# Optimization experiments

Hardware: AMD Instinct MI355X
Metric: run time of the kernel (lower is better)

## Reference

```python
import jax, jax.numpy as jnp
import numpy as np

N_ATOMS = 50000
N_EDGES = 1600000
NAB = 128   # n_atom_basis
NRBF = 20   # n_rbf
NF = 128    # n_filters

LOG2 = float(np.log(2.0))

def shifted_softplus(x):
    return jax.nn.softplus(x) - LOG2

def setup_inputs() -> dict:
    key = jax.random.key(0)
    ks = jax.random.split(key, 16)
    x = jax.random.normal(ks[0], (N_ATOMS, NAB), dtype=jnp.float32)
    f_ij = jax.random.normal(ks[1], (N_EDGES, NRBF), dtype=jnp.float32)
    rcut_ij = jax.random.uniform(ks[2], (N_EDGES,), dtype=jnp.float32)
    idx_i = jnp.sort(jax.random.randint(ks[3], (N_EDGES,), 0, N_ATOMS))
    idx_j = jax.random.randint(ks[4], (N_EDGES,), 0, N_ATOMS)
    def xavier(k, shape):
        fan_in, fan_out = shape
        s = float(np.sqrt(6.0 / (fan_in + fan_out)))
        return jax.random.uniform(k, shape, dtype=jnp.float32, minval=-s, maxval=s)
    # in2f: Dense(NAB, NF, bias=False)
    W_in2f = xavier(ks[5], (NAB, NF))
    # filter_network: Dense(NRBF, NF, act=ssp), Dense(NF, NF)
    W_f1 = xavier(ks[6], (NRBF, NF)); b_f1 = jnp.zeros((NF,), jnp.float32)
    W_f2 = xavier(ks[7], (NF, NF));   b_f2 = jnp.zeros((NF,), jnp.float32)
    # f2out: Dense(NF, NAB, act=ssp), Dense(NAB, NAB)
    W_o1 = xavier(ks[8], (NF, NAB));  b_o1 = jnp.zeros((NAB,), jnp.float32)
    W_o2 = xavier(ks[9], (NAB, NAB)); b_o2 = jnp.zeros((NAB,), jnp.float32)
    return {"x": x, "f_ij": f_ij, "rcut_ij": rcut_ij, "idx_i": idx_i, "idx_j": idx_j,
            "W_in2f": W_in2f, "W_f1": W_f1, "b_f1": b_f1, "W_f2": W_f2, "b_f2": b_f2,
            "W_o1": W_o1, "b_o1": b_o1, "W_o2": W_o2, "b_o2": b_o2}

def reference(x, f_ij, rcut_ij, idx_i, idx_j,
              W_in2f, W_f1, b_f1, W_f2, b_f2, W_o1, b_o1, W_o2, b_o2):
    # in2f (no bias, no activation): [N, NF]
    h = x @ W_in2f
    # filter network on radial basis: [E, NF]
    Wij = shifted_softplus(f_ij @ W_f1 + b_f1) @ W_f2 + b_f2
    Wij = Wij * rcut_ij[:, None]
    # cfconv: gather neighbor features, modulate by filter, scatter-sum to centers
    x_ij = h[idx_j] * Wij                      # [E, NF]
    y = jax.ops.segment_sum(x_ij, idx_i, num_segments=N_ATOMS)  # [N, NF]
    # f2out
    out = shifted_softplus(y @ W_o1 + b_o1) @ W_o2 + b_o2       # [N, NAB]
    return out
```

## Files before the change

kernel.cpp:

```cpp
#include <hip/hip_runtime.h>
#include <math.h>

#define N_ATOMS 50000
#define N_EDGES 1600000
#define NRBF 20
#define TILE_E 32
#define N_TILES (N_EDGES / TILE_E)

typedef __attribute__((ext_vector_type(8))) short bf16x8;
typedef __attribute__((ext_vector_type(4))) float f32x4;

__device__ __forceinline__ float ssp(float v) {
    const float a = fabsf(v);
    const float e = exp2f(a * -1.4426950408889634f);
    const float l = log2f(1.0f + e);
    return fmaxf(v, 0.0f) + fmaf(l, 0.6931471805599453f, -0.6931471805599453f);
}
__device__ __forceinline__ unsigned short f2bf(float f) {
    unsigned int u = __float_as_uint(f);
    u += 0x7fff + ((u >> 16) & 1);
    return (unsigned short)(u >> 16);
}
__device__ __forceinline__ float bf2f(unsigned short b) {
    return __uint_as_float(((unsigned int)b) << 16);
}
__device__ __forceinline__ void lds_barrier() {
    __asm__ __volatile__("s_waitcnt lgkmcnt(0)\ns_barrier" ::: "memory");
}

template<bool SSP_ACT, bool BIAS>
__global__ __launch_bounds__(512) void rowgemm_mfma(
    const float* __restrict__ A, const float* __restrict__ W,
    const float* __restrict__ bias, float* __restrict__ C, int nrows)
{
    const int tid  = threadIdx.x;
    const int wave = tid >> 6, lane = tid & 63;
    const int l15  = lane & 15, quad = lane >> 4;
    const int rhalf = wave >> 2, cpair = wave & 3;
    const int r0 = rhalf * 16;
    const int ntiles = (nrows + 31) >> 5;
    const int stride = gridDim.x;

    int t = blockIdx.x;
    if (t >= ntiles) return;

    float av[4][8];
    {
        const int arow0 = t * 32 + r0 + l15;
        const int arow = (arow0 < nrows) ? arow0 : (nrows - 1);
        #pragma unroll
        for (int kk = 0; kk < 4; ++kk) {
            const float4 q0 = *(const float4*)(A + (size_t)arow * 128 + kk * 32 + quad * 8);
            const float4 q1 = *(const float4*)(A + (size_t)arow * 128 + kk * 32 + quad * 8 + 4);
            av[kk][0] = q0.x; av[kk][1] = q0.y; av[kk][2] = q0.z; av[kk][3] = q0.w;
            av[kk][4] = q1.x; av[kk][5] = q1.y; av[kk][6] = q1.z; av[kk][7] = q1.w;
        }
    }

    bf16x8 wh[2][4], wl[2][4];
    float br[2];
    #pragma unroll
    for (int ct = 0; ct < 2; ++ct) {
        const int c = cpair * 32 + ct * 16 + l15;
        br[ct] = BIAS ? bias[c] : 0.0f;
        #pragma unroll
        for (int kk = 0; kk < 4; ++kk) {
            #pragma unroll
            for (int j = 0; j < 8; ++j) {
                const int k = kk * 32 + quad * 8 + j;
                const float v = W[k * 128 + c];
                const unsigned short hb = f2bf(v);
                wh[ct][kk][j] = (short)hb;
                wl[ct][kk][j] = (short)f2bf(v - bf2f(hb));
            }
        }
    }

    while (true) {
        const int tn = t + stride;
        const bool more = (tn < ntiles);
        float avn[4][8];
        if (more) {
            const int arow0 = tn * 32 + r0 + l15;
            const int arow = (arow0 < nrows) ? arow0 : (nrows - 1);
            #pragma unroll
            for (int kk = 0; kk < 4; ++kk) {
                const float4 q0 = *(const float4*)(A + (size_t)arow * 128 + kk * 32 + quad * 8);
                const float4 q1 = *(const float4*)(A + (size_t)arow * 128 + kk * 32 + quad * 8 + 4);
                avn[kk][0] = q0.x; avn[kk][1] = q0.y; avn[kk][2] = q0.z; avn[kk][3] = q0.w;
                avn[kk][4] = q1.x; avn[kk][5] = q1.y; avn[kk][6] = q1.z; avn[kk][7] = q1.w;
            }
        }
        bf16x8 ah[4], al[4];
        #pragma unroll
        for (int kk = 0; kk < 4; ++kk) {
            #pragma unroll
            for (int j = 0; j < 8; ++j) {
                const unsigned short hb = f2bf(av[kk][j]);
                ah[kk][j] = (short)hb;
                al[kk][j] = (short)f2bf(av[kk][j] - bf2f(hb));
            }
        }
        #pragma unroll
        for (int ct = 0; ct < 2; ++ct) {
            f32x4 acc = {0.0f, 0.0f, 0.0f, 0.0f};
            #pragma unroll
            for (int kk = 0; kk < 4; ++kk) {
                acc = __builtin_amdgcn_mfma_f32_16x16x32_bf16(ah[kk], wh[ct][kk], acc, 0, 0, 0);
                acc = __builtin_amdgcn_mfma_f32_16x16x32_bf16(al[kk], wh[ct][kk], acc, 0, 0, 0);
                acc = __builtin_amdgcn_mfma_f32_16x16x32_bf16(ah[kk], wl[ct][kk], acc, 0, 0, 0);
            }
            const int c = cpair * 32 + ct * 16 + l15;
            #pragma unroll
            for (int r = 0; r < 4; ++r) {
                const int row = t * 32 + r0 + quad * 4 + r;
                if (row < nrows) {
                    float v = acc[r] + br[ct];
                    if (SSP_ACT) v = ssp(v);
                    C[(size_t)row * 128 + c] = v;
                }
            }
        }
        if (!more) break;
        #pragma unroll
        for (int kk = 0; kk < 4; ++kk)
            #pragma unroll
            for (int j = 0; j < 8; ++j) av[kk][j] = avn[kk][j];
        t = tn;
    }
}

__global__ __launch_bounds__(512, 2) void edge_mfma(
    const float* __restrict__ f_ij, const float* __restrict__ rcut,
    const int* __restrict__ idx_i, const int* __restrict__ idx_j,
    const float* __restrict__ h,
    const float* __restrict__ W1, const float* __restrict__ b1,
    const float* __restrict__ W2, const float* __restrict__ b2,
    float* __restrict__ y)
{
    __shared__ unsigned short sTH[32][136];
    __shared__ float sXT[128][33];

    const int tid  = threadIdx.x;
    const int wave = tid >> 6, lane = tid & 63;
    const int l15  = lane & 15, quad = lane >> 4;
    const int rhalf = wave >> 2, cpair = wave & 3;
    const int r0  = rhalf * 16;
    const int c0  = cpair * 32 + l15;
    const int rr  = r0 + quad * 4;
    const int col = tid & 127, qtr = tid >> 7;

    bf16x8 w1h[2];
    bf16x8 w2h[2][4];
    float b1r[2], b2r[2];
    #pragma unroll
    for (int ct = 0; ct < 2; ++ct) {
        const int c = c0 + ct * 16;
        b1r[ct] = b1[c];
        b2r[ct] = b2[c];
        #pragma unroll
        for (int j = 0; j < 8; ++j) {
            const int k = quad * 8 + j;
            w1h[ct][j] = (short)f2bf((k < NRBF) ? W1[k * 128 + c] : 0.0f);
        }
        #pragma unroll
        for (int kk = 0; kk < 4; ++kk)
            #pragma unroll
            for (int j = 0; j < 8; ++j)
                w2h[ct][kk][j] = (short)f2bf(W2[(kk * 32 + quad * 8 + j) * 128 + c]);
    }

    const int nb = gridDim.x;
    const int t0 = (int)(((long long)blockIdx.x * N_TILES) / nb);
    const int t1 = (int)(((long long)(blockIdx.x + 1) * N_TILES) / nb);
    if (t0 >= t1) return;

    int   curI = idx_i[(size_t)t0 * TILE_E];
    float accV = 0.0f;

    float4 apa, apb;
    float  arc0, arc1, arc2, arc3;
    float  ahn[2][4];
    int    jn0, jn1, jn2v, jn3;

    {
        const int e0 = t0 * TILE_E;
        const float* rp = f_ij + (size_t)(e0 + r0 + l15) * NRBF;
        float4 za = {0,0,0,0}, zb = {0,0,0,0};
        if (quad < 2)       { za = *(const float4*)(rp + quad * 8); zb = *(const float4*)(rp + quad * 8 + 4); }
        else if (quad == 2) { za = *(const float4*)(rp + 16); }
        apa = za; apb = zb;
        const float4 rq = *(const float4*)(rcut + e0 + rr);
        arc0 = rq.x; arc1 = rq.y; arc2 = rq.z; arc3 = rq.w;
        const int4 j0 = *(const int4*)(idx_j + e0 + rr);
        ahn[0][0] = h[(size_t)j0.x * 128 + c0];
        ahn[0][1] = h[(size_t)j0.y * 128 + c0];
        ahn[0][2] = h[(size_t)j0.z * 128 + c0];
        ahn[0][3] = h[(size_t)j0.w * 128 + c0];
        ahn[1][0] = h[(size_t)j0.x * 128 + c0 + 16];
        ahn[1][1] = h[(size_t)j0.y * 128 + c0 + 16];
        ahn[1][2] = h[(size_t)j0.z * 128 + c0 + 16];
        ahn[1][3] = h[(size_t)j0.w * 128 + c0 + 16];
        const int tn = (t0 + 1 < N_TILES) ? t0 + 1 : N_TILES - 1;
        const int4 j1 = *(const int4*)(idx_j + tn * TILE_E + rr);
        jn0 = j1.x; jn1 = j1.y; jn2v = j1.z; jn3 = j1.w;
    }

    for (int t = t0; t < t1; ++t) {
        const int e0 = t * TILE_E;
        const int ta = (t + 1 < N_TILES) ? t + 1 : N_TILES - 1;
        const int tb = (t + 2 < N_TILES) ? t + 2 : N_TILES - 1;

        int ii[8];
        {
            const int4 i0 = *(const int4*)(idx_i + e0 + qtr * 8);
            const int4 i1 = *(const int4*)(idx_i + e0 + qtr * 8 + 4);
            ii[0] = i0.x; ii[1] = i0.y; ii[2] = i0.z; ii[3] = i0.w;
            ii[4] = i1.x; ii[5] = i1.y; ii[6] = i1.z; ii[7] = i1.w;
        }
        float4 npa = {0,0,0,0}, npb = {0,0,0,0};
        {
            const float* rp = f_ij + (size_t)(ta * TILE_E + r0 + l15) * NRBF;
            if (quad < 2)       { npa = *(const float4*)(rp + quad * 8); npb = *(const float4*)(rp + quad * 8 + 4); }
            else if (quad == 2) { npa = *(const float4*)(rp + 16); }
        }
        float nrc0, nrc1, nrc2, nrc3;
        {
            const float4 rq = *(const float4*)(rcut + ta * TILE_E + rr);
            nrc0 = rq.x; nrc1 = rq.y; nrc2 = rq.z; nrc3 = rq.w;
        }
        int j20, j21, j22, j23;
        {
            const int4 jq = *(const int4*)(idx_j + tb * TILE_E + rr);
            j20 = jq.x; j21 = jq.y; j22 = jq.z; j23 = jq.w;
        }
        float nhn[2][4];
        nhn[0][0] = h[(size_t)jn0 * 128 + c0];
        nhn[0][1] = h[(size_t)jn1 * 128 + c0];
        nhn[0][2] = h[(size_t)jn2v * 128 + c0];
        nhn[0][3] = h[(size_t)jn3 * 128 + c0];
        nhn[1][0] = h[(size_t)jn0 * 128 + c0 + 16];
        nhn[1][1] = h[(size_t)jn1 * 128 + c0 + 16];
        nhn[1][2] = h[(size_t)jn2v * 128 + c0 + 16];
        nhn[1][3] = h[(size_t)jn3 * 128 + c0 + 16];

        {
            const float va[8] = {apa.x, apa.y, apa.z, apa.w, apb.x, apb.y, apb.z, apb.w};
            bf16x8 ah, al;
            #pragma unroll
            for (int j = 0; j < 8; ++j) {
                const unsigned short hb = f2bf(va[j]);
                ah[j] = (short)hb;
                al[j] = (short)f2bf(va[j] - bf2f(hb));
            }
            #pragma unroll
            for (int ct = 0; ct < 2; ++ct) {
                f32x4 d = {0.0f, 0.0f, 0.0f, 0.0f};
                d = __builtin_amdgcn_mfma_f32_16x16x32_bf16(ah, w1h[ct], d, 0, 0, 0);
                d = __builtin_amdgcn_mfma_f32_16x16x32_bf16(al, w1h[ct], d, 0, 0, 0);
                const int c = c0 + ct * 16;
                #pragma unroll
                for (int r = 0; r < 4; ++r)
                    sTH[rr + r][c] = f2bf(ssp(d[r] + b1r[ct]));
            }
        }
        lds_barrier();

        {
            bf16x8 ath[4];
            #pragma unroll
            for (int kk = 0; kk < 4; ++kk)
                ath[kk] = *(const bf16x8*)(&sTH[r0 + l15][kk * 32 + quad * 8]);
            const float arcv[4] = {arc0, arc1, arc2, arc3};
            #pragma unroll
            for (int ct = 0; ct < 2; ++ct) {
                f32x4 acc = {0.0f, 0.0f, 0.0f, 0.0f};
                #pragma unroll
                for (int kk = 0; kk < 4; ++kk)
                    acc = __builtin_amdgcn_mfma_f32_16x16x32_bf16(ath[kk], w2h[ct][kk], acc, 0, 0, 0);
                const int c = c0 + ct * 16;
                #pragma unroll
                for (int r = 0; r < 4; ++r) {
                    const float wij = (acc[r] + b2r[ct]) * arcv[r];
                    sXT[c][rr + r] = wij * ahn[ct][r];
                }
            }
        }
        lds_barrier();

        #pragma unroll
        for (int r = 0; r < 8; ++r) {
            const float v = sXT[col][qtr * 8 + r];
            const int i = ii[r];
            if (i != curI) {
                atomicAdd(&y[(size_t)curI * 128 + col], accV);
                curI = i; accV = v;
            } else accV += v;
        }

        apa = npa; apb = npb;
        arc0 = nrc0; arc1 = nrc1; arc2 = nrc2; arc3 = nrc3;
        #pragma unroll
        for (int ct = 0; ct < 2; ++ct)
            #pragma unroll
            for (int r = 0; r < 4; ++r) ahn[ct][r] = nhn[ct][r];
        jn0 = j20; jn1 = j21; jn2v = j22; jn3 = j23;
    }
    atomicAdd(&y[(size_t)curI * 128 + col], accV);
}

extern "C" void kernel_launch(void* const* d_in, const int* in_sizes, int n_in,
                              void* d_out, int out_size, void* d_ws, size_t ws_size,
                              hipStream_t stream) {
    const float* x      = (const float*)d_in[0];
    const float* f_ij   = (const float*)d_in[1];
    const float* rcut   = (const float*)d_in[2];
    const int*   idx_i  = (const int*)d_in[3];
    const int*   idx_j  = (const int*)d_in[4];
    const float* W_in2f = (const float*)d_in[5];
    const float* W_f1   = (const float*)d_in[6];
    const float* b_f1   = (const float*)d_in[7];
    const float* W_f2   = (const float*)d_in[8];
    const float* b_f2   = (const float*)d_in[9];
    const float* W_o1   = (const float*)d_in[10];
    const float* b_o1   = (const float*)d_in[11];
    const float* W_o2   = (const float*)d_in[12];
    const float* b_o2   = (const float*)d_in[13];

    float* out = (float*)d_out;
    float* h   = (float*)d_ws;

    hipMemsetAsync(out, 0, (size_t)N_ATOMS * 128 * sizeof(float), stream);

    rowgemm_mfma<false, false><<<512, 512, 0, stream>>>(x, W_in2f, nullptr, h, N_ATOMS);
    edge_mfma<<<1024, 512, 0, stream>>>(f_ij, rcut, idx_i, idx_j, h,
                                        W_f1, b_f1, W_f2, b_f2, out);
    rowgemm_mfma<true, true><<<512, 512, 0, stream>>>(out, W_o1, b_o1, h, N_ATOMS);
    rowgemm_mfma<false, true><<<512, 512, 0, stream>>>(h, W_o2, b_o2, out, N_ATOMS);
}
```

Measured before the change: 697.5 us.

## Stage rowgemm bf16 split via LDS, fold softplus shift into bias, tweak edge grid

In the row GEMM kernels, each thread now loads the A tile coalesced, converts it once to a hi/lo bf16 pair, and stores it in LDS. Each wave then reads MFMA fragments from LDS instead of redundantly converting per-wave register copies. The edge kernel drops the -log2 shift from the first filter activation and folds it into the second-layer bias as b2 - log2 * colsum(W2_bf16). It also uses 32-bit precomputed gather offsets and a 768-block grid instead of 1024. These changes cut conversion ALU work and 64-bit address math, at the cost of extra barriers and LDS traffic in the GEMMs.

```diff
diff --git a/kernel.cpp b/kernel.cpp
--- a/kernel.cpp
+++ b/kernel.cpp
@@ -8,13 +8,17 @@
 #define N_TILES (N_EDGES / TILE_E)
 
 typedef __attribute__((ext_vector_type(8))) short bf16x8;
+typedef __attribute__((ext_vector_type(4))) short s16x4;
 typedef __attribute__((ext_vector_type(4))) float f32x4;
 
-__device__ __forceinline__ float ssp(float v) {
+__device__ __forceinline__ float sp(float v) {
     const float a = fabsf(v);
     const float e = exp2f(a * -1.4426950408889634f);
     const float l = log2f(1.0f + e);
-    return fmaxf(v, 0.0f) + fmaf(l, 0.6931471805599453f, -0.6931471805599453f);
+    return fmaxf(v, 0.0f) + l * 0.6931471805599453f;
+}
+__device__ __forceinline__ float ssp(float v) {
+    return sp(v) - 0.6931471805599453f;
 }
 __device__ __forceinline__ unsigned short f2bf(float f) {
     unsigned int u = __float_as_uint(f);
@@ -29,10 +33,13 @@
 }
 
 template<bool SSP_ACT, bool BIAS>
-__global__ __launch_bounds__(512) void rowgemm_mfma(
+__global__ __launch_bounds__(512) void rowgemm2(
     const float* __restrict__ A, const float* __restrict__ W,
     const float* __restrict__ bias, float* __restrict__ C, int nrows)
 {
+    __shared__ short sAh[32][136];
+    __shared__ short sAl[32][136];
+
     const int tid  = threadIdx.x;
     const int wave = tid >> 6, lane = tid & 63;
     const int l15  = lane & 15, quad = lane >> 4;
@@ -41,21 +48,9 @@
     const int ntiles = (nrows + 31) >> 5;
     const int stride = gridDim.x;
 
-    int t = blockIdx.x;
-    if (t >= ntiles) return;
-
-    float av[4][8];
-    {
-        const int arow0 = t * 32 + r0 + l15;
-        const int arow = (arow0 < nrows) ? arow0 : (nrows - 1);
-        #pragma unroll
-        for (int kk = 0; kk < 4; ++kk) {
-            const float4 q0 = *(const float4*)(A + (size_t)arow * 128 + kk * 32 + quad * 8);
-            const float4 q1 = *(const float4*)(A + (size_t)arow * 128 + kk * 32 + quad * 8 + 4);
-            av[kk][0] = q0.x; av[kk][1] = q0.y; av[kk][2] = q0.z; av[kk][3] = q0.w;
-            av[kk][4] = q1.x; av[kk][5] = q1.y; av[kk][6] = q1.z; av[kk][7] = q1.w;
-        }
-    }
+    const int sr0 = tid >> 5;
+    const int sr1 = sr0 + 16;
+    const int sc0 = (tid & 31) * 4;
 
     bf16x8 wh[2][4], wl[2][4];
     float br[2];
@@ -76,30 +71,47 @@
         }
     }
 
+    int t = blockIdx.x;
+    if (t >= ntiles) return;
+
+    float4 v0, v1;
+    {
+        const int ra = t * 32 + sr0, rb = t * 32 + sr1;
+        v0 = *(const float4*)(A + (size_t)((ra < nrows) ? ra : nrows - 1) * 128 + sc0);
+        v1 = *(const float4*)(A + (size_t)((rb < nrows) ? rb : nrows - 1) * 128 + sc0);
+    }
+
     while (true) {
+        {
+            const float fa[4] = {v0.x, v0.y, v0.z, v0.w};
+            const float fb[4] = {v1.x, v1.y, v1.z, v1.w};
+            s16x4 ha, la, hbv, lb;
+            #pragma unroll
+            for (int j = 0; j < 4; ++j) {
+                const unsigned short h0 = f2bf(fa[j]);
+                ha[j] = (short)h0; la[j] = (short)f2bf(fa[j] - bf2f(h0));
+                const unsigned short h1 = f2bf(fb[j]);
+                hbv[j] = (short)h1; lb[j] = (short)f2bf(fb[j] - bf2f(h1));
+            }
+            *(s16x4*)(&sAh[sr0][sc0]) = ha;  *(s16x4*)(&sAl[sr0][sc0]) = la;
+            *(s16x4*)(&sAh[sr1][sc0]) = hbv; *(s16x4*)(&sAl[sr1][sc0]) = lb;
+        }
+        __syncthreads();
+
         const int tn = t + stride;
         const bool more = (tn < ntiles);
-        float avn[4][8];
+        float4 n0, n1;
         if (more) {
-            const int arow0 = tn * 32 + r0 + l15;
-            const int arow = (arow0 < nrows) ? arow0 : (nrows - 1);
-            #pragma unroll
-            for (int kk = 0; kk < 4; ++kk) {
-                const float4 q0 = *(const float4*)(A + (size_t)arow * 128 + kk * 32 + quad * 8);
-                const float4 q1 = *(const float4*)(A + (size_t)arow * 128 + kk * 32 + quad * 8 + 4);
-                avn[kk][0] = q0.x; avn[kk][1] = q0.y; avn[kk][2] = q0.z; avn[kk][3] = q0.w;
-                avn[kk][4] = q1.x; avn[kk][5] = q1.y; avn[kk][6] = q1.z; avn[kk][7] = q1.w;
-            }
-        }
+            const int ra = tn * 32 + sr0, rb = tn * 32 + sr1;
+            n0 = *(const float4*)(A + (size_t)((ra < nrows) ? ra : nrows - 1) * 128 + sc0);
+            n1 = *(const float4*)(A + (size_t)((rb < nrows) ? rb : nrows - 1) * 128 + sc0);
+        }
+
         bf16x8 ah[4], al[4];
         #pragma unroll
         for (int kk = 0; kk < 4; ++kk) {
-            #pragma unroll
-            for (int j = 0; j < 8; ++j) {
-                const unsigned short hb = f2bf(av[kk][j]);
-                ah[kk][j] = (short)hb;
-                al[kk][j] = (short)f2bf(av[kk][j] - bf2f(hb));
-            }
+            ah[kk] = *(const bf16x8*)(&sAh[r0 + l15][kk * 32 + quad * 8]);
+            al[kk] = *(const bf16x8*)(&sAl[r0 + l15][kk * 32 + quad * 8]);
         }
         #pragma unroll
         for (int ct = 0; ct < 2; ++ct) {
@@ -122,11 +134,8 @@
             }
         }
         if (!more) break;
-        #pragma unroll
-        for (int kk = 0; kk < 4; ++kk)
-            #pragma unroll
-            for (int j = 0; j < 8; ++j) av[kk][j] = avn[kk][j];
-        t = tn;
+        __syncthreads();
+        v0 = n0; v1 = n1; t = tn;
     }
 }
 
@@ -157,17 +166,25 @@
     for (int ct = 0; ct < 2; ++ct) {
         const int c = c0 + ct * 16;
         b1r[ct] = b1[c];
-        b2r[ct] = b2[c];
         #pragma unroll
         for (int j = 0; j < 8; ++j) {
             const int k = quad * 8 + j;
             w1h[ct][j] = (short)f2bf((k < NRBF) ? W1[k * 128 + c] : 0.0f);
         }
-        #pragma unroll
-        for (int kk = 0; kk < 4; ++kk)
-            #pragma unroll
-            for (int j = 0; j < 8; ++j)
-                w2h[ct][kk][j] = (short)f2bf(W2[(kk * 32 + quad * 8 + j) * 128 + c]);
+        float csum = 0.0f;
+        #pragma unroll
+        for (int kk = 0; kk < 4; ++kk) {
+            #pragma unroll
+            for (int j = 0; j < 8; ++j) {
+                const float wv = W2[(kk * 32 + quad * 8 + j) * 128 + c];
+                const unsigned short hb = f2bf(wv);
+                w2h[ct][kk][j] = (short)hb;
+                csum += bf2f(hb);
+            }
+        }
+        csum += __shfl_xor(csum, 16);
+        csum += __shfl_xor(csum, 32);
+        b2r[ct] = b2[c] - 0.6931471805599453f * csum;
     }
 
     const int nb = gridDim.x;
@@ -193,17 +210,15 @@
         const float4 rq = *(const float4*)(rcut + e0 + rr);
         arc0 = rq.x; arc1 = rq.y; arc2 = rq.z; arc3 = rq.w;
         const int4 j0 = *(const int4*)(idx_j + e0 + rr);
-        ahn[0][0] = h[(size_t)j0.x * 128 + c0];
-        ahn[0][1] = h[(size_t)j0.y * 128 + c0];
-        ahn[0][2] = h[(size_t)j0.z * 128 + c0];
-        ahn[0][3] = h[(size_t)j0.w * 128 + c0];
-        ahn[1][0] = h[(size_t)j0.x * 128 + c0 + 16];
-        ahn[1][1] = h[(size_t)j0.y * 128 + c0 + 16];
-        ahn[1][2] = h[(size_t)j0.z * 128 + c0 + 16];
-        ahn[1][3] = h[(size_t)j0.w * 128 + c0 + 16];
+        const int o0 = j0.x * 128 + c0, o1 = j0.y * 128 + c0;
+        const int o2 = j0.z * 128 + c0, o3 = j0.w * 128 + c0;
+        ahn[0][0] = h[o0]; ahn[0][1] = h[o1]; ahn[0][2] = h[o2]; ahn[0][3] = h[o3];
+        ahn[1][0] = h[o0 + 16]; ahn[1][1] = h[o1 + 16];
+        ahn[1][2] = h[o2 + 16]; ahn[1][3] = h[o3 + 16];
         const int tn = (t0 + 1 < N_TILES) ? t0 + 1 : N_TILES - 1;
         const int4 j1 = *(const int4*)(idx_j + tn * TILE_E + rr);
-        jn0 = j1.x; jn1 = j1.y; jn2v = j1.z; jn3 = j1.w;
+        jn0 = j1.x * 128 + c0; jn1 = j1.y * 128 + c0;
+        jn2v = j1.z * 128 + c0; jn3 = j1.w * 128 + c0;
     }
 
     for (int t = t0; t < t1; ++t) {
@@ -232,17 +247,13 @@
         int j20, j21, j22, j23;
         {
             const int4 jq = *(const int4*)(idx_j + tb * TILE_E + rr);
-            j20 = jq.x; j21 = jq.y; j22 = jq.z; j23 = jq.w;
+            j20 = jq.x * 128 + c0; j21 = jq.y * 128 + c0;
+            j22 = jq.z * 128 + c0; j23 = jq.w * 128 + c0;
         }
         float nhn[2][4];
-        nhn[0][0] = h[(size_t)jn0 * 128 + c0];
-        nhn[0][1] = h[(size_t)jn1 * 128 + c0];
-        nhn[0][2] = h[(size_t)jn2v * 128 + c0];
-        nhn[0][3] = h[(size_t)jn3 * 128 + c0];
-        nhn[1][0] = h[(size_t)jn0 * 128 + c0 + 16];
-        nhn[1][1] = h[(size_t)jn1 * 128 + c0 + 16];
-        nhn[1][2] = h[(size_t)jn2v * 128 + c0 + 16];
-        nhn[1][3] = h[(size_t)jn3 * 128 + c0 + 16];
+        nhn[0][0] = h[jn0]; nhn[0][1] = h[jn1]; nhn[0][2] = h[jn2v]; nhn[0][3] = h[jn3];
+        nhn[1][0] = h[jn0 + 16]; nhn[1][1] = h[jn1 + 16];
+        nhn[1][2] = h[jn2v + 16]; nhn[1][3] = h[jn3 + 16];
 
         {
             const float va[8] = {apa.x, apa.y, apa.z, apa.w, apb.x, apb.y, apb.z, apb.w};
@@ -261,7 +272,7 @@
                 const int c = c0 + ct * 16;
                 #pragma unroll
                 for (int r = 0; r < 4; ++r)
-                    sTH[rr + r][c] = f2bf(ssp(d[r] + b1r[ct]));
+                    sTH[rr + r][c] = f2bf(sp(d[r] + b1r[ct]));
             }
         }
         lds_barrier();
@@ -293,7 +304,7 @@
             const float v = sXT[col][qtr * 8 + r];
             const int i = ii[r];
             if (i != curI) {
-                atomicAdd(&y[(size_t)curI * 128 + col], accV);
+                atomicAdd(&y[curI * 128 + col], accV);
                 curI = i; accV = v;
             } else accV += v;
         }
@@ -306,7 +317,7 @@
             for (int r = 0; r < 4; ++r) ahn[ct][r] = nhn[ct][r];
         jn0 = j20; jn1 = j21; jn2v = j22; jn3 = j23;
     }
-    atomicAdd(&y[(size_t)curI * 128 + col], accV);
+    atomicAdd(&y[curI * 128 + col], accV);
 }
 
 extern "C" void kernel_launch(void* const* d_in, const int* in_sizes, int n_in,
@@ -332,9 +343,9 @@
 
     hipMemsetAsync(out, 0, (size_t)N_ATOMS * 128 * sizeof(float), stream);
 
-    rowgemm_mfma<false, false><<<512, 512, 0, stream>>>(x, W_in2f, nullptr, h, N_ATOMS);
-    edge_mfma<<<1024, 512, 0, stream>>>(f_ij, rcut, idx_i, idx_j, h,
-                                        W_f1, b_f1, W_f2, b_f2, out);
-    rowgemm_mfma<true, true><<<512, 512, 0, stream>>>(out, W_o1, b_o1, h, N_ATOMS);
-    rowgemm_mfma<false, true><<<512, 512, 0, stream>>>(h, W_o2, b_o2, out, N_ATOMS);
-}
+    rowgemm2<false, false><<<512, 512, 0, stream>>>(x, W_in2f, nullptr, h, N_ATOMS);
+    edge_mfma<<<768, 512, 0, stream>>>(f_ij, rcut, idx_i, idx_j, h,
+                                       W_f1, b_f1, W_f2, b_f2, out);
+    rowgemm2<true, true><<<512, 512, 0, stream>>>(out, W_o1, b_o1, h, N_ATOMS);
+    rowgemm2<false, true><<<512, 512, 0, stream>>>(h, W_o2, b_o2, out, N_ATOMS);
+}
```

Result: no change. 690.2 us (-1.1%).
